# Optimization experiments

Measured on AMD Instinct MI355X. Metric: run time of the kernel, lower is better.

Reference implementation:

```python
import jax, jax.numpy as jnp
import numpy as np

FP8_E4M3_MAX = 448.0  # max finite value of float8_e4m3fn
SCALE = 2.0           # hardcoded activation scale in FP8QDQLinear.__init__
WEIGHT_SCALE = 2.0    # hardcoded weight scale


def quantize_fp8(x, scale):
    # torchao quantize_affine_float8: divide by scale, saturate to fp8 range, cast
    return jnp.clip(x / scale, -FP8_E4M3_MAX, FP8_E4M3_MAX).astype(jnp.float8_e4m3fn)


def dequantize_fp8(q, scale):
    # torchao dequantize_affine_float8: upcast to fp32 then multiply by scale
    return q.astype(jnp.float32) * scale


def setup_inputs() -> dict:
    key = jax.random.key(0)
    k1, k2, k3 = jax.random.split(key, 3)
    in_features, out_features = 4096, 4096
    inp = jax.random.normal(k1, (4, 4096, in_features), dtype=jnp.float32)
    # weight is created as randn().to(float8_e4m3fn) in __init__ (a buffer, not a Parameter)
    weight = jax.random.normal(k2, (out_features, in_features), dtype=jnp.float32).astype(jnp.float8_e4m3fn)
    bias = jax.random.normal(k3, (out_features,), dtype=jnp.float32)
    return {"input": inp, "weight": weight, "bias": bias}


def reference(input, weight, bias):
    # dequantize fp8 weight
    w = dequantize_fp8(weight, WEIGHT_SCALE)            # [O, I] fp32
    # QDQ fake-quant on activations
    dq_input = dequantize_fp8(quantize_fp8(input, SCALE), SCALE)  # [B, S, I]
    # standard linear: y = x @ W^T + b
    out = jnp.einsum('bsi,oi->bso', dq_input, w) + bias
    return out
```

## Files before the change

kernel.cpp:

```cpp
#include <hip/hip_runtime.h>

typedef float f32x4 __attribute__((ext_vector_type(4)));
typedef float f32x16 __attribute__((ext_vector_type(16)));
typedef int i32x4 __attribute__((ext_vector_type(4)));
typedef int i32x8 __attribute__((ext_vector_type(8)));

#define M_DIM 16384L
#define N_DIM 4096L
#define K_DIM 4096L

__device__ __forceinline__ unsigned int f32_to_e4m3(float x, float scale) {
  float v = fminf(fmaxf(x * scale, -448.f), 448.f);
  unsigned int u = __float_as_uint(v);
  unsigned int s = (u >> 24) & 0x80u;
  float ax = fabsf(v);
  unsigned int ua = __float_as_uint(ax);
  unsigned int subn = (unsigned int)rintf(ax * 512.0f);
  unsigned int r = ua + 0x7FFFFu + ((ua >> 20) & 1u);
  unsigned int nrm = ((r >> 20) & 0x7FFu) - 960u;
  unsigned int mag = (ax < 0.015625f) ? subn : nrm;
  return mag | s;
}

__device__ __forceinline__ unsigned int pack4_e4m3(float4 v, float scale) {
  return f32_to_e4m3(v.x, scale) | (f32_to_e4m3(v.y, scale) << 8) |
         (f32_to_e4m3(v.z, scale) << 16) | (f32_to_e4m3(v.w, scale) << 24);
}

__global__ __launch_bounds__(256) void quant_fp8(const float* __restrict__ in,
                                                 unsigned int* __restrict__ out,
                                                 float scale) {
  const long i = (long)blockIdx.x * 256 + threadIdx.x;
  out[i] = pack4_e4m3(reinterpret_cast<const float4*>(in)[i], scale);
}

__device__ __forceinline__ void gld_lds16(const unsigned char* g, unsigned char* l) {
  __builtin_amdgcn_global_load_lds(
      (const __attribute__((address_space(1))) unsigned int*)g,
      (__attribute__((address_space(3))) unsigned int*)l,
      16, 0, 0);
}

__device__ __forceinline__ uint4 quant16(const float* p, float scale) {
  const float4* q = reinterpret_cast<const float4*>(p);
  uint4 r;
  r.x = pack4_e4m3(q[0], scale);
  r.y = pack4_e4m3(q[1], scale);
  r.z = pack4_e4m3(q[2], scale);
  r.w = pack4_e4m3(q[3], scale);
  return r;
}

__device__ __forceinline__ i32x8 ldfrag(const unsigned char* p, int p_lo) {
  i32x4 lo = *reinterpret_cast<const i32x4*>(p + p_lo * 16);
  i32x4 hi = *reinterpret_cast<const i32x4*>(p + (p_lo ^ 1) * 16);
  return i32x8{lo[0], lo[1], lo[2], lo[3], hi[0], hi[1], hi[2], hi[3]};
}

#define MFMA_SC(a, b, c) \
  __builtin_amdgcn_mfma_scale_f32_32x32x64_f8f6f4((a), (b), (c), 0, 0, 0, 0x7F7F7F7F, 0, 0x7F7F7F7F)

#define BARRIER() asm volatile("s_barrier" ::: "memory")

__global__ __launch_bounds__(512, 2) void gemm_fp8_256(
    const unsigned char* __restrict__ A8, const unsigned char* __restrict__ B8,
    const float* __restrict__ bias, float* __restrict__ C) {
  __shared__ unsigned char sA[3 * 16384];
  __shared__ unsigned char sB[3 * 16384];

  const int t = threadIdx.x;
  const int lane = t & 63;
  const int w = t >> 6;
  const int wm = w >> 2;
  const int wn = w & 3;

  const int bid = (int)blockIdx.y * 16 + (int)blockIdx.x;
  const int swz = (bid & 7) * 128 + (bid >> 3);
  const long bx = swz & 15;
  const long by = swz >> 4;

  f32x16 acc[4][2] = {};

  const int sr = t >> 2;
  const int sc = (t & 3) ^ ((t >> 3) & 3);
  const unsigned char* srcA0 = A8 + (by * 256 + sr) * K_DIM + sc * 16 + 128;
  const unsigned char* srcA1 = A8 + (by * 256 + 128 + sr) * K_DIM + sc * 16 + 128;
  const unsigned char* srcB0 = B8 + (bx * 256 + sr) * K_DIM + sc * 16 + 128;
  const unsigned char* srcB1 = B8 + (bx * 256 + 128 + sr) * K_DIM + sc * 16 + 128;
  const int wofs = w * 1024;

  const int r32 = lane & 31;
  const int key = (lane >> 1) & 3;
  const int p_lo = ((lane >> 5) << 1) ^ key;
  const int arow = wm * 128 + r32;
  const int brow = wn * 64 + r32;

  gld_lds16(srcA0 - 128, sA + wofs);
  gld_lds16(srcA1 - 128, sA + 8192 + wofs);
  gld_lds16(srcB0 - 128, sB + wofs);
  gld_lds16(srcB1 - 128, sB + 8192 + wofs);
  gld_lds16(srcA0 - 64, sA + 16384 + wofs);
  gld_lds16(srcA1 - 64, sA + 16384 + 8192 + wofs);
  gld_lds16(srcB0 - 64, sB + 16384 + wofs);
  gld_lds16(srcB1 - 64, sB + 16384 + 8192 + wofs);
  asm volatile("s_waitcnt vmcnt(4)" ::: "memory");
  BARRIER();

  int b = 0;
  for (int kt = 0; kt < 64; ++kt) {
    int b2 = b + 2;
    if (b2 >= 3) b2 -= 3;
    const unsigned char* sAb = sA + b * 16384;
    const unsigned char* sBb = sB + b * 16384;
    unsigned char* dA = sA + b2 * 16384 + wofs;
    unsigned char* dB = sB + b2 * 16384 + wofs;
    const bool st = kt < 62;

    i32x8 bf0 = ldfrag(sBb + brow * 64, p_lo);
    i32x8 bf1 = ldfrag(sBb + (brow + 32) * 64, p_lo);
    i32x8 af0 = ldfrag(sAb + arow * 64, p_lo);
    i32x8 af1 = ldfrag(sAb + (arow + 32) * 64, p_lo);
    if (st) {
      gld_lds16(srcA0, dA);
      gld_lds16(srcA1, dA + 8192);
    }
    BARRIER();
    __builtin_amdgcn_s_setprio(1);
    acc[0][0] = MFMA_SC(af0, bf0, acc[0][0]);
    acc[0][1] = MFMA_SC(af0, bf1, acc[0][1]);
    acc[1][0] = MFMA_SC(af1, bf0, acc[1][0]);
    acc[1][1] = MFMA_SC(af1, bf1, acc[1][1]);
    __builtin_amdgcn_s_setprio(0);
    BARRIER();

    af0 = ldfrag(sAb + (arow + 64) * 64, p_lo);
    af1 = ldfrag(sAb + (arow + 96) * 64, p_lo);
    if (st) {
      gld_lds16(srcB0, dB);
      gld_lds16(srcB1, dB + 8192);
    }
    BARRIER();
    __builtin_amdgcn_s_setprio(1);
    acc[2][0] = MFMA_SC(af0, bf0, acc[2][0]);
    acc[2][1] = MFMA_SC(af0, bf1, acc[2][1]);
    acc[3][0] = MFMA_SC(af1, bf0, acc[3][0]);
    acc[3][1] = MFMA_SC(af1, bf1, acc[3][1]);
    __builtin_amdgcn_s_setprio(0);
    if (st) {
      asm volatile("s_waitcnt vmcnt(4)" ::: "memory");
    } else {
      asm volatile("s_waitcnt vmcnt(0)" ::: "memory");
    }
    BARRIER();

    srcA0 += 64; srcA1 += 64; srcB0 += 64; srcB1 += 64;
    if (++b == 3) b = 0;
  }

  const int mrow = 4 * (lane >> 5);
  const long gm_base = by * 256 + wm * 128;
  const long gn_base = bx * 256 + wn * 64 + r32;
#pragma unroll
  for (int nj = 0; nj < 2; ++nj) {
    const long gn = gn_base + nj * 32;
    const float bv = bias[gn];
#pragma unroll
    for (int mi = 0; mi < 4; ++mi) {
#pragma unroll
      for (int r = 0; r < 16; ++r) {
        const long gm = gm_base + mi * 32 + (r & 3) + 8 * (r >> 2) + mrow;
        C[gm * N_DIM + gn] = acc[mi][nj][r] * 4.0f + bv;
      }
    }
  }
}

template <bool FA, bool FB>
__global__ __launch_bounds__(256) void gemm_fp8_fb(const unsigned char* __restrict__ A8,
                                                   const float* __restrict__ Af,
                                                   const unsigned char* __restrict__ B8,
                                                   const float* __restrict__ Bf,
                                                   const float* __restrict__ bias,
                                                   float* __restrict__ C) {
  __shared__ unsigned char sA[128 * 64];
  __shared__ unsigned char sB[128 * 64];

  const int t = threadIdx.x;
  const int lane = t & 63;
  const int w = t >> 6;
  const int wm = w >> 1;
  const int wn = w & 1;
  const long bx = blockIdx.x;
  const long by = blockIdx.y;

  f32x16 acc[2][2] = {};

  const int l0 = w * 64 + lane;
  const int l1 = l0 + 256;
  const int r0 = l0 >> 2, c0 = (l0 & 3) ^ ((l0 >> 3) & 3);
  const int r1 = l1 >> 2, c1 = (l1 & 3) ^ ((l1 >> 3) & 3);

  const unsigned char* gA0 = nullptr; const unsigned char* gA1 = nullptr;
  const float* fA0 = nullptr;         const float* fA1 = nullptr;
  if constexpr (FA) {
    fA0 = Af + (by * 128 + r0) * K_DIM + c0 * 16;
    fA1 = Af + (by * 128 + r1) * K_DIM + c1 * 16;
  } else {
    gA0 = A8 + (by * 128 + r0) * K_DIM + c0 * 16;
    gA1 = A8 + (by * 128 + r1) * K_DIM + c1 * 16;
  }
  const unsigned char* gB0 = nullptr; const unsigned char* gB1 = nullptr;
  const float* fB0 = nullptr;         const float* fB1 = nullptr;
  if constexpr (FB) {
    fB0 = Bf + (bx * 128 + r0) * K_DIM + c0 * 16;
    fB1 = Bf + (bx * 128 + r1) * K_DIM + c1 * 16;
  } else {
    gB0 = B8 + (bx * 128 + r0) * K_DIM + c0 * 16;
    gB1 = B8 + (bx * 128 + r1) * K_DIM + c1 * 16;
  }

  unsigned char* lA0 = sA + w * 1024;
  unsigned char* lA1 = sA + 4096 + w * 1024;
  unsigned char* lB0 = sB + w * 1024;
  unsigned char* lB1 = sB + 4096 + w * 1024;

  const int r32 = lane & 31;
  const int key = (lane >> 1) & 3;
  const int p_lo = ((lane >> 5) << 1) ^ key;
  const unsigned char* sAw = sA + wm * 4096;
  const unsigned char* sBw = sB + wn * 4096;

  for (int kt = 0; kt < (int)(K_DIM / 64); ++kt) {
    if constexpr (FA) {
      *reinterpret_cast<uint4*>(sA + l0 * 16) = quant16(fA0, 0.5f);
      *reinterpret_cast<uint4*>(sA + l1 * 16) = quant16(fA1, 0.5f);
      fA0 += 64; fA1 += 64;
    } else {
      gld_lds16(gA0, lA0);
      gld_lds16(gA1, lA1);
      gA0 += 64; gA1 += 64;
    }
    if constexpr (FB) {
      *reinterpret_cast<uint4*>(sB + l0 * 16) = quant16(fB0, 1.0f);
      *reinterpret_cast<uint4*>(sB + l1 * 16) = quant16(fB1, 1.0f);
      fB0 += 64; fB1 += 64;
    } else {
      gld_lds16(gB0, lB0);
      gld_lds16(gB1, lB1);
      gB0 += 64; gB1 += 64;
    }
    __syncthreads();

    i32x8 af[2], bf[2];
#pragma unroll
    for (int i = 0; i < 2; ++i) {
      af[i] = ldfrag(sAw + (i * 32 + r32) * 64, p_lo);
      bf[i] = ldfrag(sBw + (i * 32 + r32) * 64, p_lo);
    }

#pragma unroll
    for (int i = 0; i < 2; ++i) {
#pragma unroll
      for (int j = 0; j < 2; ++j) {
        acc[i][j] = MFMA_SC(af[i], bf[j], acc[i][j]);
      }
    }
    __syncthreads();
  }

  const int mrow = 4 * (lane >> 5);
  const long gm_base = by * 128 + wm * 64;
  const long gn_base = bx * 128 + wn * 64 + r32;
#pragma unroll
  for (int nj = 0; nj < 2; ++nj) {
    const long gn = gn_base + nj * 32;
    const float bv = bias[gn];
#pragma unroll
    for (int mi = 0; mi < 2; ++mi) {
#pragma unroll
      for (int r = 0; r < 16; ++r) {
        const long gm = gm_base + mi * 32 + (r & 3) + 8 * (r >> 2) + mrow;
        C[gm * N_DIM + gn] = acc[mi][nj][r] * 4.0f + bv;
      }
    }
  }
}

extern "C" void kernel_launch(void* const* d_in, const int* in_sizes, int n_in,
                              void* d_out, int out_size, void* d_ws, size_t ws_size,
                              hipStream_t stream) {
  const float* inp = (const float*)d_in[0];
  const float* wgt = (const float*)d_in[1];
  const float* bias = (const float*)d_in[2];
  float* out = (float*)d_out;

  const size_t A_BYTES = (size_t)(M_DIM * K_DIM);
  const size_t B_BYTES = (size_t)(N_DIM * K_DIM);

  if (ws_size >= A_BYTES + B_BYTES) {
    unsigned char* aq = (unsigned char*)d_ws;
    unsigned char* wq = (unsigned char*)d_ws + A_BYTES;
    quant_fp8<<<dim3((unsigned)(M_DIM * K_DIM / 1024)), dim3(256), 0, stream>>>(
        inp, (unsigned int*)aq, 0.5f);
    quant_fp8<<<dim3((unsigned)(N_DIM * K_DIM / 1024)), dim3(256), 0, stream>>>(
        wgt, (unsigned int*)wq, 1.0f);
    gemm_fp8_256<<<dim3(16, 64), dim3(512), 0, stream>>>(aq, wq, bias, out);
  } else if (ws_size >= B_BYTES) {
    unsigned char* wq = (unsigned char*)d_ws;
    quant_fp8<<<dim3((unsigned)(N_DIM * K_DIM / 1024)), dim3(256), 0, stream>>>(
        wgt, (unsigned int*)wq, 1.0f);
    gemm_fp8_fb<true, false><<<dim3((unsigned)(N_DIM / 128), (unsigned)(M_DIM / 128)),
                               dim3(256), 0, stream>>>(nullptr, inp, wq, nullptr, bias, out);
  } else {
    gemm_fp8_fb<true, true><<<dim3((unsigned)(N_DIM / 128), (unsigned)(M_DIM / 128)),
                              dim3(256), 0, stream>>>(nullptr, inp, nullptr, wgt, bias, out);
  }
}
```

Baseline: 790.7 us.

## Shrink FP8 GEMM tile to 128x128 with 256 threads and single-phase k-loop

Replaces the 256x256 block tile (512 threads, 8 waves, two MFMA phases per k-step with four barriers) with a 128x128 tile run by 256 threads (4 waves, 2x2 wave grid, 64x64 per wave). All A and B prefetches are issued at the start of each k-step, followed by one fragment load, one MFMA group and one barrier. The block-index swizzle for L2 locality is removed. This targets more resident blocks and less barrier overhead, but halves operand reuse per byte loaded from global/LDS, so memory traffic rises.

```diff
diff --git a/kernel.cpp b/kernel.cpp
--- a/kernel.cpp
+++ b/kernel.cpp
@@ -62,47 +62,45 @@
 
 #define BARRIER() asm volatile("s_barrier" ::: "memory")
 
-__global__ __launch_bounds__(512, 2) void gemm_fp8_256(
+__global__ __launch_bounds__(256, 3) void gemm_fp8_128(
     const unsigned char* __restrict__ A8, const unsigned char* __restrict__ B8,
     const float* __restrict__ bias, float* __restrict__ C) {
-  __shared__ unsigned char sA[3 * 16384];
-  __shared__ unsigned char sB[3 * 16384];
+  __shared__ unsigned char sA[3 * 8192];
+  __shared__ unsigned char sB[3 * 8192];
 
   const int t = threadIdx.x;
   const int lane = t & 63;
   const int w = t >> 6;
-  const int wm = w >> 2;
-  const int wn = w & 3;
-
-  const int bid = (int)blockIdx.y * 16 + (int)blockIdx.x;
-  const int swz = (bid & 7) * 128 + (bid >> 3);
-  const long bx = swz & 15;
-  const long by = swz >> 4;
-
-  f32x16 acc[4][2] = {};
-
-  const int sr = t >> 2;
-  const int sc = (t & 3) ^ ((t >> 3) & 3);
-  const unsigned char* srcA0 = A8 + (by * 256 + sr) * K_DIM + sc * 16 + 128;
-  const unsigned char* srcA1 = A8 + (by * 256 + 128 + sr) * K_DIM + sc * 16 + 128;
-  const unsigned char* srcB0 = B8 + (bx * 256 + sr) * K_DIM + sc * 16 + 128;
-  const unsigned char* srcB1 = B8 + (bx * 256 + 128 + sr) * K_DIM + sc * 16 + 128;
+  const int wm = w >> 1;
+  const int wn = w & 1;
+  const long bx = blockIdx.x;
+  const long by = blockIdx.y;
+
+  f32x16 acc[2][2] = {};
+
+  const int l0 = t;
+  const int l1 = t + 256;
+  const int r0 = l0 >> 2, c0 = (l0 & 3) ^ ((l0 >> 3) & 3);
+  const int r1 = l1 >> 2, c1 = (l1 & 3) ^ ((l1 >> 3) & 3);
+
+  const unsigned char* gA0 = A8 + (by * 128 + r0) * K_DIM + c0 * 16 + 128;
+  const unsigned char* gA1 = A8 + (by * 128 + r1) * K_DIM + c1 * 16 + 128;
+  const unsigned char* gB0 = B8 + (bx * 128 + r0) * K_DIM + c0 * 16 + 128;
+  const unsigned char* gB1 = B8 + (bx * 128 + r1) * K_DIM + c1 * 16 + 128;
   const int wofs = w * 1024;
 
   const int r32 = lane & 31;
   const int key = (lane >> 1) & 3;
   const int p_lo = ((lane >> 5) << 1) ^ key;
-  const int arow = wm * 128 + r32;
-  const int brow = wn * 64 + r32;
-
-  gld_lds16(srcA0 - 128, sA + wofs);
-  gld_lds16(srcA1 - 128, sA + 8192 + wofs);
-  gld_lds16(srcB0 - 128, sB + wofs);
-  gld_lds16(srcB1 - 128, sB + 8192 + wofs);
-  gld_lds16(srcA0 - 64, sA + 16384 + wofs);
-  gld_lds16(srcA1 - 64, sA + 16384 + 8192 + wofs);
-  gld_lds16(srcB0 - 64, sB + 16384 + wofs);
-  gld_lds16(srcB1 - 64, sB + 16384 + 8192 + wofs);
+
+  gld_lds16(gA0 - 128, sA + wofs);
+  gld_lds16(gA1 - 128, sA + 4096 + wofs);
+  gld_lds16(gB0 - 128, sB + wofs);
+  gld_lds16(gB1 - 128, sB + 4096 + wofs);
+  gld_lds16(gA0 - 64, sA + 8192 + wofs);
+  gld_lds16(gA1 - 64, sA + 8192 + 4096 + wofs);
+  gld_lds16(gB0 - 64, sB + 8192 + wofs);
+  gld_lds16(gB1 - 64, sB + 8192 + 4096 + wofs);
   asm volatile("s_waitcnt vmcnt(4)" ::: "memory");
   BARRIER();
 
@@ -110,42 +108,32 @@
   for (int kt = 0; kt < 64; ++kt) {
     int b2 = b + 2;
     if (b2 >= 3) b2 -= 3;
-    const unsigned char* sAb = sA + b * 16384;
-    const unsigned char* sBb = sB + b * 16384;
-    unsigned char* dA = sA + b2 * 16384 + wofs;
-    unsigned char* dB = sB + b2 * 16384 + wofs;
     const bool st = kt < 62;
 
-    i32x8 bf0 = ldfrag(sBb + brow * 64, p_lo);
-    i32x8 bf1 = ldfrag(sBb + (brow + 32) * 64, p_lo);
-    i32x8 af0 = ldfrag(sAb + arow * 64, p_lo);
-    i32x8 af1 = ldfrag(sAb + (arow + 32) * 64, p_lo);
     if (st) {
-      gld_lds16(srcA0, dA);
-      gld_lds16(srcA1, dA + 8192);
-    }
-    BARRIER();
+      unsigned char* dA = sA + b2 * 8192 + wofs;
+      unsigned char* dB = sB + b2 * 8192 + wofs;
+      gld_lds16(gA0, dA);
+      gld_lds16(gA1, dA + 4096);
+      gld_lds16(gB0, dB);
+      gld_lds16(gB1, dB + 4096);
+      gA0 += 64; gA1 += 64; gB0 += 64; gB1 += 64;
+    }
+
+    const unsigned char* sAw = sA + b * 8192 + wm * 4096;
+    const unsigned char* sBw = sB + b * 8192 + wn * 4096;
+    i32x8 af0 = ldfrag(sAw + r32 * 64, p_lo);
+    i32x8 bf0 = ldfrag(sBw + r32 * 64, p_lo);
+    i32x8 af1 = ldfrag(sAw + (32 + r32) * 64, p_lo);
+    i32x8 bf1 = ldfrag(sBw + (32 + r32) * 64, p_lo);
+
     __builtin_amdgcn_s_setprio(1);
     acc[0][0] = MFMA_SC(af0, bf0, acc[0][0]);
     acc[0][1] = MFMA_SC(af0, bf1, acc[0][1]);
     acc[1][0] = MFMA_SC(af1, bf0, acc[1][0]);
     acc[1][1] = MFMA_SC(af1, bf1, acc[1][1]);
     __builtin_amdgcn_s_setprio(0);
-    BARRIER();
-
-    af0 = ldfrag(sAb + (arow + 64) * 64, p_lo);
-    af1 = ldfrag(sAb + (arow + 96) * 64, p_lo);
-    if (st) {
-      gld_lds16(srcB0, dB);
-      gld_lds16(srcB1, dB + 8192);
-    }
-    BARRIER();
-    __builtin_amdgcn_s_setprio(1);
-    acc[2][0] = MFMA_SC(af0, bf0, acc[2][0]);
-    acc[2][1] = MFMA_SC(af0, bf1, acc[2][1]);
-    acc[3][0] = MFMA_SC(af1, bf0, acc[3][0]);
-    acc[3][1] = MFMA_SC(af1, bf1, acc[3][1]);
-    __builtin_amdgcn_s_setprio(0);
+
     if (st) {
       asm volatile("s_waitcnt vmcnt(4)" ::: "memory");
     } else {
@@ -153,19 +141,18 @@
     }
     BARRIER();
 
-    srcA0 += 64; srcA1 += 64; srcB0 += 64; srcB1 += 64;
     if (++b == 3) b = 0;
   }
 
   const int mrow = 4 * (lane >> 5);
-  const long gm_base = by * 256 + wm * 128;
-  const long gn_base = bx * 256 + wn * 64 + r32;
+  const long gm_base = by * 128 + wm * 64;
+  const long gn_base = bx * 128 + wn * 64 + r32;
 #pragma unroll
   for (int nj = 0; nj < 2; ++nj) {
     const long gn = gn_base + nj * 32;
     const float bv = bias[gn];
 #pragma unroll
-    for (int mi = 0; mi < 4; ++mi) {
+    for (int mi = 0; mi < 2; ++mi) {
 #pragma unroll
       for (int r = 0; r < 16; ++r) {
         const long gm = gm_base + mi * 32 + (r & 3) + 8 * (r >> 2) + mrow;
@@ -304,7 +291,8 @@
         inp, (unsigned int*)aq, 0.5f);
     quant_fp8<<<dim3((unsigned)(N_DIM * K_DIM / 1024)), dim3(256), 0, stream>>>(
         wgt, (unsigned int*)wq, 1.0f);
-    gemm_fp8_256<<<dim3(16, 64), dim3(512), 0, stream>>>(aq, wq, bias, out);
+    gemm_fp8_128<<<dim3((unsigned)(N_DIM / 128), (unsigned)(M_DIM / 128)),
+                   dim3(256), 0, stream>>>(aq, wq, bias, out);
   } else if (ws_size >= B_BYTES) {
     unsigned char* wq = (unsigned char*)d_ws;
     quant_fp8<<<dim3((unsigned)(N_DIM * K_DIM / 1024)), dim3(256), 0, stream>>>(
```

Result: no change. 785.2 us (-0.7%).
